# Optimization experiments

Hardware: AMD Instinct MI355X
Metric: run time of the kernel (lower is better)

The kernel has to match this reference:

```python
import jax, jax.numpy as jnp
import numpy as np

B, S, E, L = 8, 2048, 512, 128


def setup_inputs() -> dict:
    key = jax.random.key(0)
    k1, k2 = jax.random.split(key)
    embeddings = jax.random.normal(k1, (B, S, E), dtype=jnp.float32)
    means = jax.random.normal(k2, (L, E), dtype=jnp.float32)
    var = jnp.ones((E,), dtype=jnp.float32)  # default init: requires_grad=False, ones
    return {"embeddings": embeddings, "means": means, "var": var}


def reference(embeddings, means, var):
    # Diagonal-Gaussian log-density per (token, label):
    #   log_density - 0.5 * sum_e (means[l,e] - emb[b,s,e])^2 / var[e]
    # Rewritten as GEMM + per-row/per-label norms (avoids [B,S,L,E] intermediate).
    n_embed = embeddings.shape[-1]
    factor = -n_embed / 2.0 * (np.log(2.0) + np.log(np.pi))
    # After init_params: log_density = factor - 0.5 * sum(log var); var=ones -> factor.
    log_density = factor - 0.5 * jnp.sum(jnp.log(var))
    inv_var = 1.0 / var  # [E]
    e2 = jnp.einsum('bse,e->bs', embeddings * embeddings, inv_var)      # [B,S]
    m2 = jnp.einsum('le,e->l', means * means, inv_var)                  # [L]
    cross = jnp.einsum('bse,le->bsl', embeddings, means * inv_var)      # [B,S,L]
    sq_mahalanobis = e2[..., None] + m2[None, None, :] - 2.0 * cross    # [B,S,L]
    return log_density - 0.5 * sq_mahalanobis
```

## Files before the change

### kernel.cpp

```cpp
#include <hip/hip_runtime.h>
#include <math.h>

#define BDIM 8
#define SDIM 2048
#define EDIM 512
#define LDIM 128
#define MTOT (BDIM * SDIM)
#define TM 32
#define BK 64
#define PAD 8
#define LSTR (BK + PAD)

typedef __attribute__((ext_vector_type(8))) short s8v;
typedef __attribute__((ext_vector_type(4))) float f4v;

__device__ __forceinline__ unsigned short f2bf(float x) {
    union { float f; unsigned u; } c; c.f = x;
    return (unsigned short)((c.u + 0x7fffu + ((c.u >> 16) & 1u)) >> 16);
}

__global__ __launch_bounds__(64) void gs_prep(
    const float* __restrict__ means, const float* __restrict__ var,
    unsigned short* __restrict__ Bmat, float* __restrict__ m2,
    float* __restrict__ ivbuf, float* __restrict__ coef)
{
    const int l = blockIdx.x;
    const int t = threadIdx.x;
    const int e0 = t * 8;

    float mv[8], iv[8];
    const float* mrow = means + l * EDIM + e0;
#pragma unroll
    for (int i = 0; i < 8; ++i) { mv[i] = mrow[i]; iv[i] = 1.0f / var[e0 + i]; }

    float part = 0.0f;
    s8v pr;
#pragma unroll
    for (int i = 0; i < 8; ++i) {
        float p = mv[i] * iv[i];
        pr[i] = (short)f2bf(p);
        part += mv[i] * p;
    }
    *(s8v*)(Bmat + l * EDIM + e0) = pr;

#pragma unroll
    for (int off = 32; off > 0; off >>= 1) part += __shfl_down(part, off, 64);
    if (t == 0) m2[l] = part;

    if (l == 0) {
#pragma unroll
        for (int i = 0; i < 8; ++i) ivbuf[e0 + i] = iv[i];
        float ld = 0.0f;
#pragma unroll
        for (int i = 0; i < 8; ++i) ld += logf(var[e0 + i]);
#pragma unroll
        for (int off = 32; off > 0; off >>= 1) ld += __shfl_down(ld, off, 64);
        if (t == 0) {
            const float factor = -(float)EDIM * 0.5f * 1.8378770664093453f;
            *coef = factor - 0.5f * ld;
        }
    }
}

__global__ __launch_bounds__(256) void gs_main(
    const float* __restrict__ emb, const unsigned short* __restrict__ Bmat,
    const float* __restrict__ m2, const float* __restrict__ ivbuf,
    const float* __restrict__ coef, float* __restrict__ out)
{
    __shared__ __align__(16) unsigned short Alds[TM][LSTR];
    __shared__ __align__(16) unsigned short Blds[LDIM][LSTR];
    __shared__ float e2part[256];
    __shared__ float e2s[TM];

    const int t    = threadIdx.x;
    const int lane = t & 63;
    const int wave = t >> 6;
    const int m0   = blockIdx.x * TM;

    const int arow = t >> 3;
    const int kseg = (t & 7) * 8;

    const int r0w  = (wave >> 1) * 16;
    const int c0w  = (wave & 1) * 64;
    const int frow = lane & 15;
    const int fk   = (lane >> 4) * 8;

    f4v acc[4];
#pragma unroll
    for (int i = 0; i < 4; ++i) acc[i] = (f4v)0.0f;

    float e2acc = 0.0f;
    const float* embp = emb + (m0 + arow) * EDIM + kseg;
    const unsigned short* bp = Bmat + arow * EDIM + kseg;

    for (int kc = 0; kc < EDIM / BK; ++kc) {
        const int k0 = kc * BK;
        f4v x0 = *(const f4v*)(embp + k0);
        f4v x1 = *(const f4v*)(embp + k0 + 4);
        f4v v0 = *(const f4v*)(ivbuf + k0 + kseg);
        f4v v1 = *(const f4v*)(ivbuf + k0 + kseg + 4);
        s8v b0 = *(const s8v*)(bp + (0 * 32) * EDIM + k0);
        s8v b1 = *(const s8v*)(bp + (1 * 32) * EDIM + k0);
        s8v b2 = *(const s8v*)(bp + (2 * 32) * EDIM + k0);
        s8v b3 = *(const s8v*)(bp + (3 * 32) * EDIM + k0);

        s8v a8;
#pragma unroll
        for (int i = 0; i < 4; ++i) {
            a8[i] = (short)f2bf(x0[i]);
            e2acc += x0[i] * x0[i] * v0[i];
        }
#pragma unroll
        for (int i = 0; i < 4; ++i) {
            a8[4 + i] = (short)f2bf(x1[i]);
            e2acc += x1[i] * x1[i] * v1[i];
        }

        __syncthreads();
        *(s8v*)&Alds[arow][kseg] = a8;
        *(s8v*)&Blds[arow +  0][kseg] = b0;
        *(s8v*)&Blds[arow + 32][kseg] = b1;
        *(s8v*)&Blds[arow + 64][kseg] = b2;
        *(s8v*)&Blds[arow + 96][kseg] = b3;
        __syncthreads();

#pragma unroll
        for (int ks = 0; ks < BK; ks += 32) {
            s8v af = *(const s8v*)&Alds[r0w + frow][ks + fk];
#pragma unroll
            for (int ct = 0; ct < 4; ++ct) {
                s8v bfv = *(const s8v*)&Blds[c0w + ct * 16 + frow][ks + fk];
                acc[ct] = __builtin_amdgcn_mfma_f32_16x16x32_bf16(af, bfv, acc[ct], 0, 0, 0);
            }
        }
    }

    e2part[t] = e2acc;
    __syncthreads();
    if (t < TM) {
        float s = 0.0f;
#pragma unroll
        for (int j = 0; j < 8; ++j) s += e2part[t * 8 + j];
        e2s[t] = s;
    }
    __syncthreads();

    const float cf = *coef;
#pragma unroll
    for (int ct = 0; ct < 4; ++ct) {
        const int n = c0w + ct * 16 + frow;
        const float cm = cf - 0.5f * m2[n];
#pragma unroll
        for (int r = 0; r < 4; ++r) {
            const int row = r0w + (lane >> 4) * 4 + r;
            out[(m0 + row) * LDIM + n] = acc[ct][r] + cm - 0.5f * e2s[row];
        }
    }
}

extern "C" void kernel_launch(void* const* d_in, const int* in_sizes, int n_in,
                              void* d_out, int out_size, void* d_ws, size_t ws_size,
                              hipStream_t stream) {
    const float* emb   = (const float*)d_in[0];
    const float* means = (const float*)d_in[1];
    const float* var   = (const float*)d_in[2];
    float* out = (float*)d_out;

    char* ws = (char*)d_ws;
    unsigned short* Bmat = (unsigned short*)ws;
    float* m2    = (float*)(ws + 131072);
    float* ivbuf = (float*)(ws + 131584);
    float* coef  = (float*)(ws + 133632);

    gs_prep<<<LDIM, 64, 0, stream>>>(means, var, Bmat, m2, ivbuf, coef);
    gs_main<<<MTOT / TM, 256, 0, stream>>>(emb, Bmat, m2, ivbuf, coef, out);
}
```

Baseline: 84.56 us.

## Drop LDS staging; load MFMA fragments directly from global with register prefetch

The main GEMM kernel no longer stages A and B tiles through shared memory with block barriers. Each wave now owns 16 rows and all 128 labels, loads its bf16 A fragments and B fragments straight from global memory into registers, and keeps a software prefetch ring (A four steps ahead, B two steps ahead). The e2 row-norm reduction now uses wave shuffles instead of shared memory. Removing the LDS round-trips and syncs should cut latency, at the cost of heavier register use and uncoalesced, redundant B reads from L2 across waves.

```diff
diff --git a/kernel.cpp b/kernel.cpp
--- a/kernel.cpp
+++ b/kernel.cpp
@@ -6,10 +6,6 @@
 #define EDIM 512
 #define LDIM 128
 #define MTOT (BDIM * SDIM)
-#define TM 32
-#define BK 64
-#define PAD 8
-#define LSTR (BK + PAD)
 
 typedef __attribute__((ext_vector_type(8))) short s8v;
 typedef __attribute__((ext_vector_type(4))) float f4v;
@@ -62,98 +58,98 @@
     }
 }
 
-__global__ __launch_bounds__(256) void gs_main(
+__global__ __launch_bounds__(128) void gs_main(
     const float* __restrict__ emb, const unsigned short* __restrict__ Bmat,
     const float* __restrict__ m2, const float* __restrict__ ivbuf,
     const float* __restrict__ coef, float* __restrict__ out)
 {
-    __shared__ __align__(16) unsigned short Alds[TM][LSTR];
-    __shared__ __align__(16) unsigned short Blds[LDIM][LSTR];
-    __shared__ float e2part[256];
-    __shared__ float e2s[TM];
-
     const int t    = threadIdx.x;
     const int lane = t & 63;
     const int wave = t >> 6;
-    const int m0   = blockIdx.x * TM;
+    const int q    = lane >> 4;
+    const int fr   = lane & 15;
+    const int m0   = blockIdx.x * 32 + wave * 16;
 
-    const int arow = t >> 3;
-    const int kseg = (t & 7) * 8;
+    const float*          ap  = emb   + (size_t)(m0 + fr) * EDIM + q * 8;
+    const unsigned short* bp  = Bmat  + fr * EDIM + q * 8;
+    const float*          ivp = ivbuf + q * 8;
 
-    const int r0w  = (wave >> 1) * 16;
-    const int c0w  = (wave & 1) * 64;
-    const int frow = lane & 15;
-    const int fk   = (lane >> 4) * 8;
+    f4v acc[8];
+#pragma unroll
+    for (int i = 0; i < 8; ++i) acc[i] = (f4v)0.0f;
 
-    f4v acc[4];
+    f4v a0[4], a1[4];
+    f4v v0[2], v1[2];
+    s8v bf[2][8];
+
 #pragma unroll
-    for (int i = 0; i < 4; ++i) acc[i] = (f4v)0.0f;
+    for (int p = 0; p < 4; ++p) {
+        a0[p] = *(const f4v*)(ap + 32 * p);
+        a1[p] = *(const f4v*)(ap + 32 * p + 4);
+    }
+#pragma unroll
+    for (int p = 0; p < 2; ++p) {
+        v0[p] = *(const f4v*)(ivp + 32 * p);
+        v1[p] = *(const f4v*)(ivp + 32 * p + 4);
+#pragma unroll
+        for (int ct = 0; ct < 8; ++ct)
+            bf[p][ct] = *(const s8v*)(bp + ct * 16 * EDIM + 32 * p);
+    }
 
     float e2acc = 0.0f;
-    const float* embp = emb + (m0 + arow) * EDIM + kseg;
-    const unsigned short* bp = Bmat + arow * EDIM + kseg;
 
-    for (int kc = 0; kc < EDIM / BK; ++kc) {
-        const int k0 = kc * BK;
-        f4v x0 = *(const f4v*)(embp + k0);
-        f4v x1 = *(const f4v*)(embp + k0 + 4);
-        f4v v0 = *(const f4v*)(ivbuf + k0 + kseg);
-        f4v v1 = *(const f4v*)(ivbuf + k0 + kseg + 4);
-        s8v b0 = *(const s8v*)(bp + (0 * 32) * EDIM + k0);
-        s8v b1 = *(const s8v*)(bp + (1 * 32) * EDIM + k0);
-        s8v b2 = *(const s8v*)(bp + (2 * 32) * EDIM + k0);
-        s8v b3 = *(const s8v*)(bp + (3 * 32) * EDIM + k0);
+#pragma unroll
+    for (int s = 0; s < 16; ++s) {
+        f4v xa = a0[s & 3], xb = a1[s & 3];
+        f4v va = v0[s & 1], vb = v1[s & 1];
+        s8v bcur[8];
+#pragma unroll
+        for (int ct = 0; ct < 8; ++ct) bcur[ct] = bf[s & 1][ct];
 
-        s8v a8;
+        if (s + 4 < 16) {
+            a0[(s + 4) & 3] = *(const f4v*)(ap + 32 * (s + 4));
+            a1[(s + 4) & 3] = *(const f4v*)(ap + 32 * (s + 4) + 4);
+        }
+        if (s + 2 < 16) {
+            v0[s & 1] = *(const f4v*)(ivp + 32 * (s + 2));
+            v1[s & 1] = *(const f4v*)(ivp + 32 * (s + 2) + 4);
+#pragma unroll
+            for (int ct = 0; ct < 8; ++ct)
+                bf[s & 1][ct] = *(const s8v*)(bp + ct * 16 * EDIM + 32 * (s + 2));
+        }
+
+        s8v af;
 #pragma unroll
         for (int i = 0; i < 4; ++i) {
-            a8[i] = (short)f2bf(x0[i]);
-            e2acc += x0[i] * x0[i] * v0[i];
+            af[i] = (short)f2bf(xa[i]);
+            e2acc += xa[i] * xa[i] * va[i];
         }
 #pragma unroll
         for (int i = 0; i < 4; ++i) {
-            a8[4 + i] = (short)f2bf(x1[i]);
-            e2acc += x1[i] * x1[i] * v1[i];
+            af[4 + i] = (short)f2bf(xb[i]);
+            e2acc += xb[i] * xb[i] * vb[i];
         }
 
-        __syncthreads();
-        *(s8v*)&Alds[arow][kseg] = a8;
-        *(s8v*)&Blds[arow +  0][kseg] = b0;
-        *(s8v*)&Blds[arow + 32][kseg] = b1;
-        *(s8v*)&Blds[arow + 64][kseg] = b2;
-        *(s8v*)&Blds[arow + 96][kseg] = b3;
-        __syncthreads();
-
 #pragma unroll
-        for (int ks = 0; ks < BK; ks += 32) {
-            s8v af = *(const s8v*)&Alds[r0w + frow][ks + fk];
-#pragma unroll
-            for (int ct = 0; ct < 4; ++ct) {
-                s8v bfv = *(const s8v*)&Blds[c0w + ct * 16 + frow][ks + fk];
-                acc[ct] = __builtin_amdgcn_mfma_f32_16x16x32_bf16(af, bfv, acc[ct], 0, 0, 0);
-            }
-        }
+        for (int ct = 0; ct < 8; ++ct)
+            acc[ct] = __builtin_amdgcn_mfma_f32_16x16x32_bf16(af, bcur[ct], acc[ct], 0, 0, 0);
     }
 
-    e2part[t] = e2acc;
-    __syncthreads();
-    if (t < TM) {
-        float s = 0.0f;
+    e2acc += __shfl_xor(e2acc, 16, 64);
+    e2acc += __shfl_xor(e2acc, 32, 64);
+    float e2row[4];
 #pragma unroll
-        for (int j = 0; j < 8; ++j) s += e2part[t * 8 + j];
-        e2s[t] = s;
-    }
-    __syncthreads();
+    for (int r = 0; r < 4; ++r) e2row[r] = __shfl(e2acc, q * 4 + r, 64);
 
     const float cf = *coef;
 #pragma unroll
-    for (int ct = 0; ct < 4; ++ct) {
-        const int n = c0w + ct * 16 + frow;
+    for (int ct = 0; ct < 8; ++ct) {
+        const int n = ct * 16 + fr;
         const float cm = cf - 0.5f * m2[n];
 #pragma unroll
         for (int r = 0; r < 4; ++r) {
-            const int row = r0w + (lane >> 4) * 4 + r;
-            out[(m0 + row) * LDIM + n] = acc[ct][r] + cm - 0.5f * e2s[row];
+            const int row = q * 4 + r;
+            out[(size_t)(m0 + row) * LDIM + n] = acc[ct][r] + cm - 0.5f * e2row[r];
         }
     }
 }
@@ -173,5 +169,5 @@
     float* coef  = (float*)(ws + 133632);
 
     gs_prep<<<LDIM, 64, 0, stream>>>(means, var, Bmat, m2, ivbuf, coef);
-    gs_main<<<MTOT / TM, 256, 0, stream>>>(emb, Bmat, m2, ivbuf, coef, out);
+    gs_main<<<MTOT / 32, 128, 0, stream>>>(emb, Bmat, m2, ivbuf, coef, out);
 }
```

Measured after the change: 94.75 us. 1.12x slower.

## Double-buffer LDS and prefetch embeddings with async global-to-LDS loads for means

Applied to the files above, without the earlier changes.

Rewrites the main GEMM loop as a software pipeline. LDS is double-buffered and only one barrier is used per k-step. Embedding and inverse-variance registers are loaded two stages ahead. The bf16 means tile is staged with global_load_lds directly into LDS in MFMA fragment order, so it no longer passes through registers. The aim is to hide global-load latency behind MFMA work and cut synchronization. The cost is doubled LDS use and extra registers, plus reliance on the compiler inserting the correct wait before the barrier for the async LDS loads.

```diff
diff --git a/kernel.cpp b/kernel.cpp
--- a/kernel.cpp
+++ b/kernel.cpp
@@ -1,15 +1,12 @@
 #include <hip/hip_runtime.h>
 #include <math.h>
 
-#define BDIM 8
-#define SDIM 2048
 #define EDIM 512
 #define LDIM 128
-#define MTOT (BDIM * SDIM)
+#define MTOT 16384
 #define TM 32
 #define BK 64
-#define PAD 8
-#define LSTR (BK + PAD)
+#define LSTR 72
 
 typedef __attribute__((ext_vector_type(8))) short s8v;
 typedef __attribute__((ext_vector_type(4))) float f4v;
@@ -17,6 +14,12 @@
 __device__ __forceinline__ unsigned short f2bf(float x) {
     union { float f; unsigned u; } c; c.f = x;
     return (unsigned short)((c.u + 0x7fffu + ((c.u >> 16) & 1u)) >> 16);
+}
+
+__device__ __forceinline__ void ld_lds16(const void* g, void* l) {
+    __builtin_amdgcn_global_load_lds(
+        (const __attribute__((address_space(1))) unsigned int*)g,
+        (__attribute__((address_space(3))) unsigned int*)l, 16, 0, 0);
 }
 
 __global__ __launch_bounds__(64) void gs_prep(
@@ -67,69 +70,85 @@
     const float* __restrict__ m2, const float* __restrict__ ivbuf,
     const float* __restrict__ coef, float* __restrict__ out)
 {
-    __shared__ __align__(16) unsigned short Alds[TM][LSTR];
-    __shared__ __align__(16) unsigned short Blds[LDIM][LSTR];
+    __shared__ __align__(16) unsigned short Alds[2][TM][LSTR];
+    __shared__ __align__(16) unsigned short Blds[2][16 * 64 * 8];
     __shared__ float e2part[256];
     __shared__ float e2s[TM];
 
     const int t    = threadIdx.x;
     const int lane = t & 63;
-    const int wave = t >> 6;
+    const int w    = t >> 6;
+    const int q    = lane >> 4;
+    const int fr   = lane & 15;
     const int m0   = blockIdx.x * TM;
 
     const int arow = t >> 3;
     const int kseg = (t & 7) * 8;
 
-    const int r0w  = (wave >> 1) * 16;
-    const int c0w  = (wave & 1) * 64;
-    const int frow = lane & 15;
-    const int fk   = (lane >> 4) * 8;
+    const int r0w = (w >> 1) * 16;
+    const int c0w1 = (w & 1) * 4;
+
+    const float* ap  = emb   + (size_t)(m0 + arow) * EDIM + kseg;
+    const float* ivp = ivbuf + kseg;
 
     f4v acc[4];
 #pragma unroll
     for (int i = 0; i < 4; ++i) acc[i] = (f4v)0.0f;
+    float e2acc = 0.0f;
 
-    float e2acc = 0.0f;
-    const float* embp = emb + (m0 + arow) * EDIM + kseg;
-    const unsigned short* bp = Bmat + arow * EDIM + kseg;
+    f4v ar0[2], ar1[2], vr0[2], vr1[2];
+    ar0[0] = *(const f4v*)(ap);          ar1[0] = *(const f4v*)(ap + 4);
+    ar0[1] = *(const f4v*)(ap + BK);     ar1[1] = *(const f4v*)(ap + BK + 4);
+    vr0[0] = *(const f4v*)(ivp);         vr1[0] = *(const f4v*)(ivp + 4);
+    vr0[1] = *(const f4v*)(ivp + BK);    vr1[1] = *(const f4v*)(ivp + BK + 4);
 
+#define STAGE_B(kc, buf)                                                        \
+    {                                                                           \
+        _Pragma("unroll")                                                       \
+        for (int j = 0; j < 4; ++j) {                                           \
+            const int F   = w * 4 + j;                                          \
+            const int col = (F & 7) * 16 + fr;                                  \
+            const int kk  = (kc) * BK + (F >> 3) * 32 + q * 8;                  \
+            ld_lds16(Bmat + col * EDIM + kk, (void*)&Blds[buf][F * 512]);       \
+        }                                                                       \
+    }
+
+    STAGE_B(0, 0)
+
+#pragma unroll
     for (int kc = 0; kc < EDIM / BK; ++kc) {
-        const int k0 = kc * BK;
-        f4v x0 = *(const f4v*)(embp + k0);
-        f4v x1 = *(const f4v*)(embp + k0 + 4);
-        f4v v0 = *(const f4v*)(ivbuf + k0 + kseg);
-        f4v v1 = *(const f4v*)(ivbuf + k0 + kseg + 4);
-        s8v b0 = *(const s8v*)(bp + (0 * 32) * EDIM + k0);
-        s8v b1 = *(const s8v*)(bp + (1 * 32) * EDIM + k0);
-        s8v b2 = *(const s8v*)(bp + (2 * 32) * EDIM + k0);
-        s8v b3 = *(const s8v*)(bp + (3 * 32) * EDIM + k0);
+        const int b = kc & 1;
 
+        f4v xa = ar0[b], xb = ar1[b], va = vr0[b], vb = vr1[b];
         s8v a8;
 #pragma unroll
         for (int i = 0; i < 4; ++i) {
-            a8[i] = (short)f2bf(x0[i]);
-            e2acc += x0[i] * x0[i] * v0[i];
+            a8[i] = (short)f2bf(xa[i]);
+            e2acc += xa[i] * xa[i] * va[i];
         }
 #pragma unroll
         for (int i = 0; i < 4; ++i) {
-            a8[4 + i] = (short)f2bf(x1[i]);
-            e2acc += x1[i] * x1[i] * v1[i];
+            a8[4 + i] = (short)f2bf(xb[i]);
+            e2acc += xb[i] * xb[i] * vb[i];
+        }
+        *(s8v*)&Alds[b][arow][kseg] = a8;
+
+        __syncthreads();
+
+        if (kc + 1 < EDIM / BK) STAGE_B(kc + 1, b ^ 1)
+        if (kc + 2 < EDIM / BK) {
+            const int k2 = (kc + 2) * BK;
+            ar0[b] = *(const f4v*)(ap + k2);  ar1[b] = *(const f4v*)(ap + k2 + 4);
+            vr0[b] = *(const f4v*)(ivp + k2); vr1[b] = *(const f4v*)(ivp + k2 + 4);
         }
 
-        __syncthreads();
-        *(s8v*)&Alds[arow][kseg] = a8;
-        *(s8v*)&Blds[arow +  0][kseg] = b0;
-        *(s8v*)&Blds[arow + 32][kseg] = b1;
-        *(s8v*)&Blds[arow + 64][kseg] = b2;
-        *(s8v*)&Blds[arow + 96][kseg] = b3;
-        __syncthreads();
-
 #pragma unroll
-        for (int ks = 0; ks < BK; ks += 32) {
-            s8v af = *(const s8v*)&Alds[r0w + frow][ks + fk];
+        for (int ks_i = 0; ks_i < 2; ++ks_i) {
+            s8v af = *(const s8v*)&Alds[b][r0w + fr][ks_i * 32 + q * 8];
 #pragma unroll
             for (int ct = 0; ct < 4; ++ct) {
-                s8v bfv = *(const s8v*)&Blds[c0w + ct * 16 + frow][ks + fk];
+                const int F = ks_i * 8 + c0w1 + ct;
+                s8v bfv = *(const s8v*)&Blds[b][F * 512 + lane * 8];
                 acc[ct] = __builtin_amdgcn_mfma_f32_16x16x32_bf16(af, bfv, acc[ct], 0, 0, 0);
             }
         }
@@ -148,14 +167,15 @@
     const float cf = *coef;
 #pragma unroll
     for (int ct = 0; ct < 4; ++ct) {
-        const int n = c0w + ct * 16 + frow;
+        const int n = (c0w1 + ct) * 16 + fr;
         const float cm = cf - 0.5f * m2[n];
 #pragma unroll
         for (int r = 0; r < 4; ++r) {
-            const int row = r0w + (lane >> 4) * 4 + r;
-            out[(m0 + row) * LDIM + n] = acc[ct][r] + cm - 0.5f * e2s[row];
+            const int row = r0w + q * 4 + r;
+            out[(size_t)(m0 + row) * LDIM + n] = acc[ct][r] + cm - 0.5f * e2s[row];
         }
     }
+#undef STAGE_B
 }
 
 extern "C" void kernel_launch(void* const* d_in, const int* in_sizes, int n_in,
```

Result: slower. 90.14 us (+6.6%).
